# Optimization experiments

Hardware: AMD Instinct MI355X
Metric: run time of the kernel (lower is better)

The kernel has to match this reference:

```python
import jax, jax.numpy as jnp
import numpy as np

DIM = 768
HEADS = 12
HEAD_DIM = 64
INNER = HEADS * HEAD_DIM  # 768


def setup_inputs() -> dict:
    key = jax.random.key(0)
    k_x, k_wqkv, k_bqkv, k_wout, k_bout = jax.random.split(key, 5)
    B, S = 2, 2048
    x = jax.random.normal(k_x, (B, S, DIM), dtype=jnp.float32)
    # nn.Linear(dim, 3*inner): weight [out, in]; store transposed for x @ W
    lim = 1.0 / np.sqrt(DIM)
    w_qkv = jax.random.uniform(k_wqkv, (DIM, 3 * INNER), minval=-lim, maxval=lim, dtype=jnp.float32)
    b_qkv = jax.random.uniform(k_bqkv, (3 * INNER,), minval=-lim, maxval=lim, dtype=jnp.float32)
    lim2 = 1.0 / np.sqrt(INNER)
    # original zero-inits to_out; use random weights so the reference output is non-trivial
    w_out = jax.random.uniform(k_wout, (INNER, DIM), minval=-lim2, maxval=lim2, dtype=jnp.float32)
    b_out = jax.random.uniform(k_bout, (DIM,), minval=-lim2, maxval=lim2, dtype=jnp.float32)
    return {"x": x, "w_qkv": w_qkv, "b_qkv": b_qkv, "w_out": w_out, "b_out": b_out}


def reference(x, w_qkv, b_qkv, w_out, b_out):
    B, S, _ = x.shape
    qkv = x @ w_qkv + b_qkv                               # [B, S, 3*H*D]
    qkv = qkv.reshape(B, S, 3, HEADS, HEAD_DIM)           # b s three h d
    q, k, v = qkv[:, :, 0], qkv[:, :, 1], qkv[:, :, 2]    # each [B, S, H, D]
    scale = 1.0 / np.sqrt(HEAD_DIM)
    # non-causal self-attention (FlashSelfAttention, dropout=0, causal=False)
    scores = jnp.einsum('bshd,bthd->bhst', q, k) * scale  # [B, H, S, S]
    attn = jax.nn.softmax(scores, axis=-1)
    ctx = jnp.einsum('bhst,bthd->bshd', attn, v)          # [B, S, H, D]
    ctx = ctx.reshape(B, S, INNER)
    return ctx @ w_out + b_out                            # [B, S, DIM]
```

## Files before the change

### kernel.cpp

```cpp
#include <hip/hip_runtime.h>
#include <cstddef>
#include <cstdint>

#define DIM  768
#define NH   12
#define HD   64
#define SEQ  2048
#define NB   2
#define NQKV 2304
#define G    (NB * NH * SEQ)

typedef _Float16 f16x8 __attribute__((ext_vector_type(8)));
typedef _Float16 f16x4 __attribute__((ext_vector_type(4)));
typedef float    f32x4 __attribute__((ext_vector_type(4)));
typedef float    f32x16 __attribute__((ext_vector_type(16)));

#if __has_builtin(__builtin_amdgcn_exp2f)
#define EXP2(x) __builtin_amdgcn_exp2f(x)
#else
#define EXP2(x) exp2f(x)
#endif

#define QSCALE 0.1803368801111244f
#define C2     6.0f

__device__ __forceinline__ void gld16(const _Float16* g, _Float16* l) {
  __builtin_amdgcn_global_load_lds(
      (const __attribute__((address_space(1))) void*)g,
      (__attribute__((address_space(3))) void*)l, 16, 0, 0);
}

__global__ __launch_bounds__(256) void transpose_cvt_kernel(
    const float* __restrict__ W, _Float16* __restrict__ WT, int K, int N) {
  __shared__ _Float16 tl[32][36];
  const int t = threadIdx.x;
  const int k0 = blockIdx.y * 32, n0 = blockIdx.x * 32;
  {
    const int r = t >> 3, c4 = (t & 7) * 4;
    float4 f = *(const float4*)(W + (size_t)(k0 + r) * N + n0 + c4);
    tl[r][c4 + 0] = (_Float16)f.x; tl[r][c4 + 1] = (_Float16)f.y;
    tl[r][c4 + 2] = (_Float16)f.z; tl[r][c4 + 3] = (_Float16)f.w;
  }
  __syncthreads();
  const int n = t >> 3, kc = (t & 7) * 4;
  f16x4 v;
  v[0] = tl[kc + 0][n]; v[1] = tl[kc + 1][n];
  v[2] = tl[kc + 2][n]; v[3] = tl[kc + 3][n];
  *(f16x4*)(WT + (size_t)(n0 + n) * K + k0 + kc) = v;
}

__global__ __launch_bounds__(256) void vtrans_kernel(
    const _Float16* __restrict__ v, _Float16* __restrict__ vT) {
  __shared__ _Float16 tl[64][68];
  const int t = threadIdx.x;
  const int bh = blockIdx.x, st = blockIdx.y;
  const size_t base = (size_t)bh * SEQ * HD;
  {
    const int s = t >> 2, dc = (t & 3) * 16;
    const _Float16* p = v + base + (size_t)(st * 64 + s) * HD + dc;
    f16x8 a = *(const f16x8*)p, b = *(const f16x8*)(p + 8);
    *(f16x8*)&tl[s][dc] = a;
    *(f16x8*)&tl[s][dc + 8] = b;
  }
  __syncthreads();
  const int d = t >> 2, sc = (t & 3) * 16;
  f16x8 o0, o1;
#pragma unroll
  for (int j = 0; j < 8; j++) { o0[j] = tl[sc + j][d]; o1[j] = tl[sc + 8 + j][d]; }
  _Float16* q = vT + base + (size_t)d * SEQ + st * 64 + sc;
  *(f16x8*)q = o0;
  *(f16x8*)(q + 8) = o1;
}

__global__ __launch_bounds__(256) void qkv_gemm_kernel(
    const float* __restrict__ X, const _Float16* __restrict__ BT,
    const float* __restrict__ bias, _Float16* __restrict__ q,
    _Float16* __restrict__ k, _Float16* __restrict__ v) {
  __shared__ _Float16 As[128 * 32];
  __shared__ _Float16 Bs[128 * 32];
  const int tid = threadIdx.x;
  const int lane = tid & 63, wv = tid >> 6;
  const int wm = wv >> 1, wn = wv & 1;
  const int quad = lane >> 4, lcol = lane & 15;
  const int bm = blockIdx.y * 128, bn = blockIdx.x * 128;
  const int K = DIM, N = NQKV;

  f32x4 acc[4][4];
#pragma unroll
  for (int i = 0; i < 4; i++)
#pragma unroll
    for (int j = 0; j < 4; j++) acc[i][j] = (f32x4)(0.f);

  const float* asrc[2];
  _Float16* adst[2];
#pragma unroll
  for (int i = 0; i < 2; i++) {
    const int rA = 64 * i + (tid >> 2);
    const int cc = tid & 3;
    asrc[i] = X + (size_t)(bm + rA) * K + cc * 8;
    adst[i] = As + rA * 32 + ((cc ^ ((rA >> 1) & 3)) * 8);
  }
  const int r0 = wv * 32 + (lane >> 2);
  const int kp = (((lane & 3) ^ ((r0 >> 1) & 3)) * 8);
  const _Float16* b0p = BT + (size_t)(bn + r0) * K + kp;
  const _Float16* b1p = BT + (size_t)(bn + r0 + 16) * K + kp;
  _Float16* lB0 = Bs + (wv * 2 + 0) * 512;
  _Float16* lB1 = Bs + (wv * 2 + 1) * 512;

  for (int k0 = 0; k0 < K; k0 += 32) {
    float4 a0[2], a1[2];
#pragma unroll
    for (int i = 0; i < 2; i++) {
      a0[i] = *(const float4*)(asrc[i] + k0);
      a1[i] = *(const float4*)(asrc[i] + k0 + 4);
    }
    __syncthreads();
    gld16(b0p + k0, lB0);
    gld16(b1p + k0, lB1);
#pragma unroll
    for (int i = 0; i < 2; i++) {
      f16x8 h;
      h[0] = (_Float16)a0[i].x; h[1] = (_Float16)a0[i].y;
      h[2] = (_Float16)a0[i].z; h[3] = (_Float16)a0[i].w;
      h[4] = (_Float16)a1[i].x; h[5] = (_Float16)a1[i].y;
      h[6] = (_Float16)a1[i].z; h[7] = (_Float16)a1[i].w;
      *(f16x8*)adst[i] = h;
    }
    __syncthreads();

    f16x8 af[4], bf[4];
#pragma unroll
    for (int mi = 0; mi < 4; mi++) {
      const int R = wm * 64 + mi * 16 + lcol;
      af[mi] = *(const f16x8*)&As[R * 32 + ((quad ^ ((R >> 1) & 3)) * 8)];
    }
#pragma unroll
    for (int ni = 0; ni < 4; ni++) {
      const int R = wn * 64 + ni * 16 + lcol;
      bf[ni] = *(const f16x8*)&Bs[R * 32 + ((quad ^ ((R >> 1) & 3)) * 8)];
    }
#pragma unroll
    for (int mi = 0; mi < 4; mi++)
#pragma unroll
      for (int ni = 0; ni < 4; ni++)
        acc[mi][ni] = __builtin_amdgcn_mfma_f32_16x16x32_f16(af[mi], bf[ni], acc[mi][ni], 0, 0, 0);
  }

#pragma unroll
  for (int mi = 0; mi < 4; mi++) {
#pragma unroll
    for (int r = 0; r < 4; r++) {
      const int row = bm + wm * 64 + mi * 16 + quad * 4 + r;
      const int b_ = row >> 11, s_ = row & 2047;
#pragma unroll
      for (int ni = 0; ni < 4; ni++) {
        const int c = bn + wn * 64 + ni * 16 + lcol;
        const float val = acc[mi][ni][r] + bias[c];
        const int d = c & 63;
        const int which = c / 768;
        const int h = (c - which * 768) >> 6;
        const size_t idx = (((size_t)b_ * NH + h) * SEQ + s_) * HD + d;
        if (which == 0)      q[idx] = (_Float16)(val * QSCALE);
        else if (which == 1) k[idx] = (_Float16)val;
        else                 v[idx] = (_Float16)val;
      }
    }
  }
}

#define PST 68
__global__ __launch_bounds__(256) void attn_part_kernel(
    const _Float16* __restrict__ Q, const _Float16* __restrict__ K,
    const _Float16* __restrict__ V, _Float16* __restrict__ Ohat,
    float* __restrict__ L) {
  __shared__ _Float16 Ks[64 * PST];
  __shared__ _Float16 Vs[64 * PST];
  __shared__ _Float16 Ps[128 * PST];
  const int tid = threadIdx.x, lane = tid & 63, wv = tid >> 6;
  const int lr = lane & 31, hw = lane >> 5;
  const int bh = blockIdx.x, qt = blockIdx.y, ks = blockIdx.z;
  const size_t base = (size_t)bh * SEQ * HD;

  f16x8 qb[4];
  {
    const _Float16* qp = Q + base + (size_t)(qt * 128 + wv * 32 + lr) * HD + hw * 8;
#pragma unroll
    for (int f = 0; f < 4; f++) qb[f] = *(const f16x8*)(qp + f * 16);
  }

  f32x16 o0 = (f32x16)(0.f), o1 = (f32x16)(0.f);
  float l_part = 0.f;

  const int sr = tid >> 2;
  const int sc = (tid & 3) * 16;
  const _Float16* Kb = K + base + (size_t)ks * (SEQ / 2) * HD;
  const _Float16* Vb = V + base + ks * (SEQ / 2);

  for (int t = 0; t < (SEQ / 2) / 64; t++) {
    const _Float16* kp = Kb + (size_t)(t * 64 + sr) * HD + sc;
    f16x8 k0v = *(const f16x8*)kp, k1v = *(const f16x8*)(kp + 8);
    const _Float16* vp = Vb + (size_t)sr * SEQ + t * 64 + sc;
    f16x8 v0v = *(const f16x8*)vp, v1v = *(const f16x8*)(vp + 8);

    __syncthreads();
    *(f16x8*)&Ks[sr * PST + sc] = k0v;
    *(f16x8*)&Ks[sr * PST + sc + 8] = k1v;
    *(f16x8*)&Vs[sr * PST + sc] = v0v;
    *(f16x8*)&Vs[sr * PST + sc + 8] = v1v;
    __syncthreads();

    f32x16 s0 = (f32x16)(0.f), s1 = (f32x16)(0.f);
#pragma unroll
    for (int f = 0; f < 4; f++) {
      f16x8 ka0 = *(const f16x8*)&Ks[(lr) * PST + f * 16 + hw * 8];
      f16x8 ka1 = *(const f16x8*)&Ks[(32 + lr) * PST + f * 16 + hw * 8];
      s0 = __builtin_amdgcn_mfma_f32_32x32x16_f16(ka0, qb[f], s0, 0, 0, 0);
      s1 = __builtin_amdgcn_mfma_f32_32x32x16_f16(ka1, qb[f], s1, 0, 0, 0);
    }

    _Float16* pw = &Ps[(size_t)(wv * 32 + lr) * PST];
#pragma unroll
    for (int rg = 0; rg < 4; rg++) {
      f16x4 pk0, pk1;
#pragma unroll
      for (int i = 0; i < 4; i++) {
        const float p0 = EXP2(s0[rg * 4 + i] - C2);
        const float p1 = EXP2(s1[rg * 4 + i] - C2);
        l_part += p0 + p1;
        pk0[i] = (_Float16)p0;
        pk1[i] = (_Float16)p1;
      }
      *(f16x4*)&pw[0  + 8 * rg + 4 * hw] = pk0;
      *(f16x4*)&pw[32 + 8 * rg + 4 * hw] = pk1;
    }

#pragma unroll
    for (int f = 0; f < 4; f++) {
      f16x8 pa  = *(const f16x8*)&Ps[(size_t)(wv * 32 + lr) * PST + f * 16 + hw * 8];
      f16x8 vb0 = *(const f16x8*)&Vs[(lr) * PST + f * 16 + hw * 8];
      f16x8 vb1 = *(const f16x8*)&Vs[(32 + lr) * PST + f * 16 + hw * 8];
      o0 = __builtin_amdgcn_mfma_f32_32x32x16_f16(pa, vb0, o0, 0, 0, 0);
      o1 = __builtin_amdgcn_mfma_f32_32x32x16_f16(pa, vb1, o1, 0, 0, 0);
    }
  }

  const float l_full = l_part + __shfl_xor(l_part, 32);
  __syncthreads();
  float* lsh = (float*)&Ps[(size_t)(wv * 32) * PST];
  if (hw == 0) lsh[lr] = l_full;
  __syncthreads();

  const size_t rbase = (size_t)ks * G + (size_t)bh * SEQ + qt * 128 + wv * 32;
  if (hw == 0) L[rbase + lr] = l_full;
  float linv[16];
#pragma unroll
  for (int r = 0; r < 16; r++)
    linv[r] = 1.0f / lsh[(r & 3) + 8 * (r >> 2) + 4 * hw];
#pragma unroll
  for (int r = 0; r < 16; r++) {
    const int rr = (r & 3) + 8 * (r >> 2) + 4 * hw;
    _Float16* cp = Ohat + (rbase + rr) * HD;
    cp[lr]      = (_Float16)(o0[r] * linv[r]);
    cp[32 + lr] = (_Float16)(o1[r] * linv[r]);
  }
}

__global__ __launch_bounds__(256) void out_gemm_kernel(
    const _Float16* __restrict__ Ohat, const float* __restrict__ L,
    const _Float16* __restrict__ WT, const float* __restrict__ bias,
    float* __restrict__ out) {
  __shared__ _Float16 As[64 * 36];
  __shared__ _Float16 Bs[64 * 36];
  const int tid = threadIdx.x, lane = tid & 63, wv = tid >> 6;
  const int wr = (wv >> 1) * 32, wc = (wv & 1) * 32;
  const int quad = lane >> 4, lcol = lane & 15;
  const int bm = blockIdx.y * 64, bn = blockIdx.x * 64;

  f32x4 acc[2][2];
#pragma unroll
  for (int i = 0; i < 2; i++)
#pragma unroll
    for (int j = 0; j < 2; j++) acc[i][j] = (f32x4)(0.f);

  const int ra = tid >> 2, ca = (tid & 3) * 8;
  const int grow = bm + ra, b_ = grow >> 11, s_ = grow & 2047;

  for (int k0 = 0; k0 < DIM; k0 += 32) {
    const int h = k0 >> 6;
    const int lidx = (b_ * NH + h) * SEQ + s_;
    const size_t obase = (size_t)lidx * HD + (k0 & 32) + ca;
    f16x8 u0 = *(const f16x8*)(Ohat + obase);
    f16x8 u1 = *(const f16x8*)(Ohat + (size_t)G * HD + obase);
    const float l0 = L[lidx], l1 = L[G + lidx];
    const float w0 = l0 / (l0 + l1), w1 = 1.0f - w0;
    f16x8 bv = *(const f16x8*)(WT + (size_t)(bn + ra) * DIM + k0 + ca);

    __syncthreads();
    f16x8 av;
#pragma unroll
    for (int j = 0; j < 8; j++)
      av[j] = (_Float16)(w0 * (float)u0[j] + w1 * (float)u1[j]);
    *(f16x8*)&As[ra * 36 + ca] = av;
    *(f16x8*)&Bs[ra * 36 + ca] = bv;
    __syncthreads();

    f16x8 af[2], bf[2];
#pragma unroll
    for (int mi = 0; mi < 2; mi++)
      af[mi] = *(const f16x8*)&As[(wr + mi * 16 + lcol) * 36 + quad * 8];
#pragma unroll
    for (int ni = 0; ni < 2; ni++)
      bf[ni] = *(const f16x8*)&Bs[(wc + ni * 16 + lcol) * 36 + quad * 8];
#pragma unroll
    for (int mi = 0; mi < 2; mi++)
#pragma unroll
      for (int ni = 0; ni < 2; ni++)
        acc[mi][ni] = __builtin_amdgcn_mfma_f32_16x16x32_f16(af[mi], bf[ni], acc[mi][ni], 0, 0, 0);
  }

#pragma unroll
  for (int mi = 0; mi < 2; mi++) {
#pragma unroll
    for (int r = 0; r < 4; r++) {
      const int row = bm + wr + mi * 16 + quad * 4 + r;
#pragma unroll
      for (int ni = 0; ni < 2; ni++) {
        const int col = bn + wc + ni * 16 + lcol;
        out[(size_t)row * DIM + col] = acc[mi][ni][r] + bias[col];
      }
    }
  }
}

extern "C" void kernel_launch(void* const* d_in, const int* in_sizes, int n_in,
                              void* d_out, int out_size, void* d_ws,
                              size_t ws_size, hipStream_t stream) {
  const float* x = (const float*)d_in[0];
  const float* w_qkv = (const float*)d_in[1];
  const float* b_qkv = (const float*)d_in[2];
  const float* w_out = (const float*)d_in[3];
  const float* b_out = (const float*)d_in[4];
  float* out = (float*)d_out;

  _Float16* wsh = (_Float16*)d_ws;
  size_t off = 0;
  const size_t hsz = (size_t)NB * NH * SEQ * HD;
  _Float16* wqkvT = wsh + off; off += (size_t)NQKV * DIM;
  _Float16* woutT = wsh + off; off += (size_t)DIM * DIM;
  _Float16* qh   = wsh + off; off += hsz;
  _Float16* kh   = wsh + off; off += hsz;
  _Float16* vh   = wsh + off; off += hsz;
  _Float16* vT   = wsh + off; off += hsz;
  _Float16* Ohat = wsh + off; off += 2 * hsz;
  float*    Lbuf = (float*)(wsh + off);

  transpose_cvt_kernel<<<dim3(NQKV / 32, DIM / 32), 256, 0, stream>>>(w_qkv, wqkvT, DIM, NQKV);
  transpose_cvt_kernel<<<dim3(DIM / 32, DIM / 32), 256, 0, stream>>>(w_out, woutT, DIM, DIM);
  qkv_gemm_kernel<<<dim3(NQKV / 128, (NB * SEQ) / 128), 256, 0, stream>>>(
      x, wqkvT, b_qkv, qh, kh, vh);
  vtrans_kernel<<<dim3(NB * NH, SEQ / 64), 256, 0, stream>>>(vh, vT);
  attn_part_kernel<<<dim3(NB * NH, SEQ / 128, 2), 256, 0, stream>>>(
      qh, kh, vT, Ohat, Lbuf);
  out_gemm_kernel<<<dim3(DIM / 64, (NB * SEQ) / 64), 256, 0, stream>>>(
      Ohat, Lbuf, woutT, b_out, out);
}
```

Before: 178.7 us.

## Restructure attention: 64-row query tiles per wave, 4-way key split, separate merge

The QKV GEMM epilogue now writes V directly in transposed layout, which removes the separate V-transpose kernel. The attention kernel gives each wave 64 query rows (two 32-row subtiles), so every K/V tile loaded into LDS is reused for twice as many queries, and the key dimension is split four ways. A new merge kernel combines the four partial outputs into a contiguous fp16 context buffer. The output GEMM then loads that buffer with direct global-to-LDS loads into a swizzled layout instead of merging inline. The cost is an extra launch and more partial-output traffic, plus higher register use in the attention kernel. That kernel also now has half as many query blocks in exchange for four key splits.

```diff
diff --git a/kernel.cpp b/kernel.cpp
--- a/kernel.cpp
+++ b/kernel.cpp
@@ -9,6 +9,8 @@
 #define NB   2
 #define NQKV 2304
 #define G    (NB * NH * SEQ)
+#define KSPLIT 4
+#define KPS  (SEQ / KSPLIT)
 
 typedef _Float16 f16x8 __attribute__((ext_vector_type(8)));
 typedef _Float16 f16x4 __attribute__((ext_vector_type(4)));
@@ -47,29 +49,6 @@
   v[0] = tl[kc + 0][n]; v[1] = tl[kc + 1][n];
   v[2] = tl[kc + 2][n]; v[3] = tl[kc + 3][n];
   *(f16x4*)(WT + (size_t)(n0 + n) * K + k0 + kc) = v;
-}
-
-__global__ __launch_bounds__(256) void vtrans_kernel(
-    const _Float16* __restrict__ v, _Float16* __restrict__ vT) {
-  __shared__ _Float16 tl[64][68];
-  const int t = threadIdx.x;
-  const int bh = blockIdx.x, st = blockIdx.y;
-  const size_t base = (size_t)bh * SEQ * HD;
-  {
-    const int s = t >> 2, dc = (t & 3) * 16;
-    const _Float16* p = v + base + (size_t)(st * 64 + s) * HD + dc;
-    f16x8 a = *(const f16x8*)p, b = *(const f16x8*)(p + 8);
-    *(f16x8*)&tl[s][dc] = a;
-    *(f16x8*)&tl[s][dc + 8] = b;
-  }
-  __syncthreads();
-  const int d = t >> 2, sc = (t & 3) * 16;
-  f16x8 o0, o1;
-#pragma unroll
-  for (int j = 0; j < 8; j++) { o0[j] = tl[sc + j][d]; o1[j] = tl[sc + 8 + j][d]; }
-  _Float16* q = vT + base + (size_t)d * SEQ + st * 64 + sc;
-  *(f16x8*)q = o0;
-  *(f16x8*)(q + 8) = o1;
 }
 
 __global__ __launch_bounds__(256) void qkv_gemm_kernel(
@@ -83,7 +62,7 @@
   const int wm = wv >> 1, wn = wv & 1;
   const int quad = lane >> 4, lcol = lane & 15;
   const int bm = blockIdx.y * 128, bn = blockIdx.x * 128;
-  const int K = DIM, N = NQKV;
+  const int K = DIM;
 
   f32x4 acc[4][4];
 #pragma unroll
@@ -159,10 +138,12 @@
         const int d = c & 63;
         const int which = c / 768;
         const int h = (c - which * 768) >> 6;
-        const size_t idx = (((size_t)b_ * NH + h) * SEQ + s_) * HD + d;
-        if (which == 0)      q[idx] = (_Float16)(val * QSCALE);
-        else if (which == 1) k[idx] = (_Float16)val;
-        else                 v[idx] = (_Float16)val;
+        if (which == 0)
+          q[(((size_t)b_ * NH + h) * SEQ + s_) * HD + d] = (_Float16)(val * QSCALE);
+        else if (which == 1)
+          k[(((size_t)b_ * NH + h) * SEQ + s_) * HD + d] = (_Float16)val;
+        else
+          v[(((size_t)b_ * NH + h) * HD + d) * SEQ + s_] = (_Float16)val;
       }
     }
   }
@@ -175,28 +156,35 @@
     float* __restrict__ L) {
   __shared__ _Float16 Ks[64 * PST];
   __shared__ _Float16 Vs[64 * PST];
-  __shared__ _Float16 Ps[128 * PST];
+  __shared__ _Float16 Ps[4 * 64 * PST];
   const int tid = threadIdx.x, lane = tid & 63, wv = tid >> 6;
   const int lr = lane & 31, hw = lane >> 5;
   const int bh = blockIdx.x, qt = blockIdx.y, ks = blockIdx.z;
   const size_t base = (size_t)bh * SEQ * HD;
 
-  f16x8 qb[4];
-  {
-    const _Float16* qp = Q + base + (size_t)(qt * 128 + wv * 32 + lr) * HD + hw * 8;
-#pragma unroll
-    for (int f = 0; f < 4; f++) qb[f] = *(const f16x8*)(qp + f * 16);
-  }
-
-  f32x16 o0 = (f32x16)(0.f), o1 = (f32x16)(0.f);
-  float l_part = 0.f;
+  f16x8 qb[2][4];
+#pragma unroll
+  for (int sub = 0; sub < 2; sub++) {
+    const _Float16* qp =
+        Q + base + (size_t)(qt * 256 + wv * 64 + sub * 32 + lr) * HD + hw * 8;
+#pragma unroll
+    for (int f = 0; f < 4; f++) qb[sub][f] = *(const f16x8*)(qp + f * 16);
+  }
+
+  f32x16 o[2][2];
+#pragma unroll
+  for (int i = 0; i < 2; i++)
+#pragma unroll
+    for (int j = 0; j < 2; j++) o[i][j] = (f32x16)(0.f);
+  float lp[2] = {0.f, 0.f};
 
   const int sr = tid >> 2;
   const int sc = (tid & 3) * 16;
-  const _Float16* Kb = K + base + (size_t)ks * (SEQ / 2) * HD;
-  const _Float16* Vb = V + base + ks * (SEQ / 2);
-
-  for (int t = 0; t < (SEQ / 2) / 64; t++) {
+  const _Float16* Kb = K + base + (size_t)ks * KPS * HD;
+  const _Float16* Vb = V + base + ks * KPS;
+  _Float16* Pw = &Ps[(size_t)wv * 64 * PST];
+
+  for (int t = 0; t < KPS / 64; t++) {
     const _Float16* kp = Kb + (size_t)(t * 64 + sr) * HD + sc;
     f16x8 k0v = *(const f16x8*)kp, k1v = *(const f16x8*)(kp + 8);
     const _Float16* vp = Vb + (size_t)sr * SEQ + t * 64 + sc;
@@ -209,68 +197,105 @@
     *(f16x8*)&Vs[sr * PST + sc + 8] = v1v;
     __syncthreads();
 
-    f32x16 s0 = (f32x16)(0.f), s1 = (f32x16)(0.f);
+    f32x16 s[2][2];
+#pragma unroll
+    for (int i = 0; i < 2; i++)
+#pragma unroll
+      for (int j = 0; j < 2; j++) s[i][j] = (f32x16)(0.f);
 #pragma unroll
     for (int f = 0; f < 4; f++) {
       f16x8 ka0 = *(const f16x8*)&Ks[(lr) * PST + f * 16 + hw * 8];
       f16x8 ka1 = *(const f16x8*)&Ks[(32 + lr) * PST + f * 16 + hw * 8];
-      s0 = __builtin_amdgcn_mfma_f32_32x32x16_f16(ka0, qb[f], s0, 0, 0, 0);
-      s1 = __builtin_amdgcn_mfma_f32_32x32x16_f16(ka1, qb[f], s1, 0, 0, 0);
-    }
-
-    _Float16* pw = &Ps[(size_t)(wv * 32 + lr) * PST];
-#pragma unroll
-    for (int rg = 0; rg < 4; rg++) {
-      f16x4 pk0, pk1;
-#pragma unroll
-      for (int i = 0; i < 4; i++) {
-        const float p0 = EXP2(s0[rg * 4 + i] - C2);
-        const float p1 = EXP2(s1[rg * 4 + i] - C2);
-        l_part += p0 + p1;
-        pk0[i] = (_Float16)p0;
-        pk1[i] = (_Float16)p1;
+      s[0][0] = __builtin_amdgcn_mfma_f32_32x32x16_f16(ka0, qb[0][f], s[0][0], 0, 0, 0);
+      s[0][1] = __builtin_amdgcn_mfma_f32_32x32x16_f16(ka1, qb[0][f], s[0][1], 0, 0, 0);
+      s[1][0] = __builtin_amdgcn_mfma_f32_32x32x16_f16(ka0, qb[1][f], s[1][0], 0, 0, 0);
+      s[1][1] = __builtin_amdgcn_mfma_f32_32x32x16_f16(ka1, qb[1][f], s[1][1], 0, 0, 0);
+    }
+
+#pragma unroll
+    for (int sub = 0; sub < 2; sub++) {
+      _Float16* pw = Pw + (size_t)(sub * 32 + lr) * PST;
+#pragma unroll
+      for (int rg = 0; rg < 4; rg++) {
+        f16x4 pk0, pk1;
+#pragma unroll
+        for (int i = 0; i < 4; i++) {
+          const float p0 = EXP2(s[sub][0][rg * 4 + i] - C2);
+          const float p1 = EXP2(s[sub][1][rg * 4 + i] - C2);
+          lp[sub] += p0 + p1;
+          pk0[i] = (_Float16)p0;
+          pk1[i] = (_Float16)p1;
+        }
+        *(f16x4*)&pw[0  + 8 * rg + 4 * hw] = pk0;
+        *(f16x4*)&pw[32 + 8 * rg + 4 * hw] = pk1;
       }
-      *(f16x4*)&pw[0  + 8 * rg + 4 * hw] = pk0;
-      *(f16x4*)&pw[32 + 8 * rg + 4 * hw] = pk1;
     }
 
 #pragma unroll
     for (int f = 0; f < 4; f++) {
-      f16x8 pa  = *(const f16x8*)&Ps[(size_t)(wv * 32 + lr) * PST + f * 16 + hw * 8];
       f16x8 vb0 = *(const f16x8*)&Vs[(lr) * PST + f * 16 + hw * 8];
       f16x8 vb1 = *(const f16x8*)&Vs[(32 + lr) * PST + f * 16 + hw * 8];
-      o0 = __builtin_amdgcn_mfma_f32_32x32x16_f16(pa, vb0, o0, 0, 0, 0);
-      o1 = __builtin_amdgcn_mfma_f32_32x32x16_f16(pa, vb1, o1, 0, 0, 0);
-    }
-  }
-
-  const float l_full = l_part + __shfl_xor(l_part, 32);
-  __syncthreads();
-  float* lsh = (float*)&Ps[(size_t)(wv * 32) * PST];
-  if (hw == 0) lsh[lr] = l_full;
-  __syncthreads();
-
-  const size_t rbase = (size_t)ks * G + (size_t)bh * SEQ + qt * 128 + wv * 32;
-  if (hw == 0) L[rbase + lr] = l_full;
-  float linv[16];
-#pragma unroll
-  for (int r = 0; r < 16; r++)
-    linv[r] = 1.0f / lsh[(r & 3) + 8 * (r >> 2) + 4 * hw];
-#pragma unroll
-  for (int r = 0; r < 16; r++) {
-    const int rr = (r & 3) + 8 * (r >> 2) + 4 * hw;
-    _Float16* cp = Ohat + (rbase + rr) * HD;
-    cp[lr]      = (_Float16)(o0[r] * linv[r]);
-    cp[32 + lr] = (_Float16)(o1[r] * linv[r]);
-  }
+      f16x8 pa0 = *(const f16x8*)&Pw[(size_t)(lr) * PST + f * 16 + hw * 8];
+      f16x8 pa1 = *(const f16x8*)&Pw[(size_t)(32 + lr) * PST + f * 16 + hw * 8];
+      o[0][0] = __builtin_amdgcn_mfma_f32_32x32x16_f16(pa0, vb0, o[0][0], 0, 0, 0);
+      o[0][1] = __builtin_amdgcn_mfma_f32_32x32x16_f16(pa0, vb1, o[0][1], 0, 0, 0);
+      o[1][0] = __builtin_amdgcn_mfma_f32_32x32x16_f16(pa1, vb0, o[1][0], 0, 0, 0);
+      o[1][1] = __builtin_amdgcn_mfma_f32_32x32x16_f16(pa1, vb1, o[1][1], 0, 0, 0);
+    }
+  }
+
+  float* lsh = (float*)Pw;
+#pragma unroll
+  for (int sub = 0; sub < 2; sub++) {
+    const float l_full = lp[sub] + __shfl_xor(lp[sub], 32);
+    if (hw == 0) lsh[sub * 32 + lr] = l_full;
+    const size_t rbase =
+        (size_t)ks * G + (size_t)bh * SEQ + qt * 256 + wv * 64 + sub * 32;
+    if (hw == 0) L[rbase + lr] = l_full;
+#pragma unroll
+    for (int r = 0; r < 16; r++) {
+      const int rr = (r & 3) + 8 * (r >> 2) + 4 * hw;
+      const float linv = 1.0f / lsh[sub * 32 + rr];
+      _Float16* cp = Ohat + (rbase + rr) * HD;
+      cp[lr]      = (_Float16)(o[sub][0][r] * linv);
+      cp[32 + lr] = (_Float16)(o[sub][1][r] * linv);
+    }
+  }
+}
+
+__global__ __launch_bounds__(256) void attn_merge_kernel(
+    const _Float16* __restrict__ Ohat, const float* __restrict__ L,
+    _Float16* __restrict__ ctx) {
+  const size_t gid = (size_t)blockIdx.x * 256 + threadIdx.x;
+  const int row = (int)(gid >> 3);
+  const int dp = ((int)gid & 7) * 8;
+  float lv[KSPLIT], lsum = 0.f;
+#pragma unroll
+  for (int s = 0; s < KSPLIT; s++) { lv[s] = L[(size_t)s * G + row]; lsum += lv[s]; }
+  const float inv = 1.0f / lsum;
+  float acc[8];
+#pragma unroll
+  for (int j = 0; j < 8; j++) acc[j] = 0.f;
+#pragma unroll
+  for (int s = 0; s < KSPLIT; s++) {
+    const float w = lv[s] * inv;
+    f16x8 a = *(const f16x8*)(Ohat + ((size_t)s * G + row) * HD + dp);
+#pragma unroll
+    for (int j = 0; j < 8; j++) acc[j] += w * (float)a[j];
+  }
+  const int bh = row >> 11, s_ = row & 2047;
+  const int b_ = bh / NH, h_ = bh % NH;
+  f16x8 o8;
+#pragma unroll
+  for (int j = 0; j < 8; j++) o8[j] = (_Float16)acc[j];
+  *(f16x8*)(ctx + ((size_t)b_ * SEQ + s_) * DIM + h_ * HD + dp) = o8;
 }
 
 __global__ __launch_bounds__(256) void out_gemm_kernel(
-    const _Float16* __restrict__ Ohat, const float* __restrict__ L,
-    const _Float16* __restrict__ WT, const float* __restrict__ bias,
-    float* __restrict__ out) {
-  __shared__ _Float16 As[64 * 36];
-  __shared__ _Float16 Bs[64 * 36];
+    const _Float16* __restrict__ A, const _Float16* __restrict__ WT,
+    const float* __restrict__ bias, float* __restrict__ out) {
+  __shared__ _Float16 As[64 * 32];
+  __shared__ _Float16 Bs[64 * 32];
   const int tid = threadIdx.x, lane = tid & 63, wv = tid >> 6;
   const int wr = (wv >> 1) * 32, wc = (wv & 1) * 32;
   const int quad = lane >> 4, lcol = lane & 15;
@@ -282,35 +307,30 @@
 #pragma unroll
     for (int j = 0; j < 2; j++) acc[i][j] = (f32x4)(0.f);
 
-  const int ra = tid >> 2, ca = (tid & 3) * 8;
-  const int grow = bm + ra, b_ = grow >> 11, s_ = grow & 2047;
+  const int r0 = wv * 16 + (lane >> 2);
+  const int kp = (((lane & 3) ^ ((r0 >> 1) & 3)) * 8);
+  const _Float16* asrc = A + (size_t)(bm + r0) * DIM + kp;
+  const _Float16* bsrc = WT + (size_t)(bn + r0) * DIM + kp;
+  _Float16* adst = As + wv * 16 * 32;
+  _Float16* bdst = Bs + wv * 16 * 32;
 
   for (int k0 = 0; k0 < DIM; k0 += 32) {
-    const int h = k0 >> 6;
-    const int lidx = (b_ * NH + h) * SEQ + s_;
-    const size_t obase = (size_t)lidx * HD + (k0 & 32) + ca;
-    f16x8 u0 = *(const f16x8*)(Ohat + obase);
-    f16x8 u1 = *(const f16x8*)(Ohat + (size_t)G * HD + obase);
-    const float l0 = L[lidx], l1 = L[G + lidx];
-    const float w0 = l0 / (l0 + l1), w1 = 1.0f - w0;
-    f16x8 bv = *(const f16x8*)(WT + (size_t)(bn + ra) * DIM + k0 + ca);
-
-    __syncthreads();
-    f16x8 av;
-#pragma unroll
-    for (int j = 0; j < 8; j++)
-      av[j] = (_Float16)(w0 * (float)u0[j] + w1 * (float)u1[j]);
-    *(f16x8*)&As[ra * 36 + ca] = av;
-    *(f16x8*)&Bs[ra * 36 + ca] = bv;
+    __syncthreads();
+    gld16(asrc + k0, adst);
+    gld16(bsrc + k0, bdst);
     __syncthreads();
 
     f16x8 af[2], bf[2];
 #pragma unroll
-    for (int mi = 0; mi < 2; mi++)
-      af[mi] = *(const f16x8*)&As[(wr + mi * 16 + lcol) * 36 + quad * 8];
-#pragma unroll
-    for (int ni = 0; ni < 2; ni++)
-      bf[ni] = *(const f16x8*)&Bs[(wc + ni * 16 + lcol) * 36 + quad * 8];
+    for (int mi = 0; mi < 2; mi++) {
+      const int R = wr + mi * 16 + lcol;
+      af[mi] = *(const f16x8*)&As[R * 32 + ((quad ^ ((R >> 1) & 3)) * 8)];
+    }
+#pragma unroll
+    for (int ni = 0; ni < 2; ni++) {
+      const int R = wc + ni * 16 + lcol;
+      bf[ni] = *(const f16x8*)&Bs[R * 32 + ((quad ^ ((R >> 1) & 3)) * 8)];
+    }
 #pragma unroll
     for (int mi = 0; mi < 2; mi++)
 #pragma unroll
@@ -349,18 +369,18 @@
   _Float16* woutT = wsh + off; off += (size_t)DIM * DIM;
   _Float16* qh   = wsh + off; off += hsz;
   _Float16* kh   = wsh + off; off += hsz;
-  _Float16* vh   = wsh + off; off += hsz;
   _Float16* vT   = wsh + off; off += hsz;
-  _Float16* Ohat = wsh + off; off += 2 * hsz;
+  _Float16* Ohat = wsh + off; off += (size_t)KSPLIT * hsz;
   float*    Lbuf = (float*)(wsh + off);
+  _Float16* ctxh = qh;
 
   transpose_cvt_kernel<<<dim3(NQKV / 32, DIM / 32), 256, 0, stream>>>(w_qkv, wqkvT, DIM, NQKV);
   transpose_cvt_kernel<<<dim3(DIM / 32, DIM / 32), 256, 0, stream>>>(w_out, woutT, DIM, DIM);
   qkv_gemm_kernel<<<dim3(NQKV / 128, (NB * SEQ) / 128), 256, 0, stream>>>(
-      x, wqkvT, b_qkv, qh, kh, vh);
-  vtrans_kernel<<<dim3(NB * NH, SEQ / 64), 256, 0, stream>>>(vh, vT);
-  attn_part_kernel<<<dim3(NB * NH, SEQ / 128, 2), 256, 0, stream>>>(
+      x, wqkvT, b_qkv, qh, kh, vT);
+  attn_part_kernel<<<dim3(NB * NH, SEQ / 256, KSPLIT), 256, 0, stream>>>(
       qh, kh, vT, Ohat, Lbuf);
+  attn_merge_kernel<<<(G * HD) / (256 * 8), 256, 0, stream>>>(Ohat, Lbuf, ctxh);
   out_gemm_kernel<<<dim3(DIM / 64, (NB * SEQ) / 64), 256, 0, stream>>>(
-      Ohat, Lbuf, woutT, b_out, out);
-}
+      ctxh, woutT, b_out, out);
+}
```

Result: slower. 213.0 us (+19.2%).
